# Optimization experiments

Measured on AMD Instinct MI355X. Metric: run time of the kernel, lower is better.

## Reference

```python
import jax, jax.numpy as jnp
import numpy as np
from functools import reduce

N_QUBITS = 6
DIM = 2 ** N_QUBITS  # 64

# PauliZ expectation signs per wire: zsign[j, q] = +1 if bit q of basis state j is 0 else -1
# PennyLane convention: wire 0 is the most-significant bit.
_ZSIGN = jnp.asarray(1.0 - 2.0 * ((np.arange(DIM)[:, None] >> (N_QUBITS - 1 - np.arange(N_QUBITS))[None, :]) & 1), dtype=jnp.float32)  # [64, 6]

def _cnot_perm(c, t):
    # permutation p with new_state[j] = old_state[p[j]] for CNOT(control=c, target=t)
    idx = np.arange(DIM)
    cbit = (idx >> (N_QUBITS - 1 - c)) & 1
    return idx ^ (cbit << (N_QUBITS - 1 - t))

def _ring_perm(r):
    # compose the ring of CNOTs: CNOT(w, (w+r)%n) for w = 0..n-1 applied in order
    total = np.arange(DIM)
    for w in range(N_QUBITS):
        total = total[_cnot_perm(w, (w + r) % N_QUBITS)]
    return total

_RING = {r: jnp.asarray(_ring_perm(r)) for r in (1, 2)}

def _rot(phi, theta, omega):
    # PennyLane Rot(phi, theta, omega) = RZ(omega) @ RY(theta) @ RZ(phi)
    c = jnp.cos(theta / 2.0)
    s = jnp.sin(theta / 2.0)
    em = jnp.exp(-0.5j * (phi + omega))
    ep = jnp.exp(0.5j * (phi - omega))
    return jnp.stack([jnp.stack([em * c, -ep * s]),
                      jnp.stack([jnp.conj(ep) * s, jnp.conj(em) * c])])

def _strongly_entangling(psi, theta):
    # theta: [L, N_QUBITS, 3]; psi: [B, 64] complex
    L = theta.shape[0]
    for l in range(L):
        mats = [_rot(theta[l, w, 0], theta[l, w, 1], theta[l, w, 2]) for w in range(N_QUBITS)]
        U = reduce(jnp.kron, mats)  # [64, 64]; wire 0 = most significant, matches kron order
        psi = psi @ U.T
        r = l % (N_QUBITS - 1) + 1  # PennyLane default ranges
        psi = psi[:, _RING[r]]
    return psi

def setup_inputs() -> dict:
    key = jax.random.key(0)
    ks = jax.random.split(key, 12)
    B, D, H, NW = 131072, 64, 64, 5
    return {
        'x': jax.random.normal(ks[0], (B, D), dtype=jnp.float32),
        'W1': jax.random.normal(ks[1], (H, D), dtype=jnp.float32) * 0.1,
        'b1': jnp.zeros((H,), dtype=jnp.float32),
        'ln_g': jnp.ones((H,), dtype=jnp.float32),
        'ln_b': jnp.zeros((H,), dtype=jnp.float32),
        'W2': jax.random.normal(ks[2], (N_QUBITS, H), dtype=jnp.float32) * 0.1,
        'b2': jnp.zeros((N_QUBITS,), dtype=jnp.float32),
        'theta_shared': jax.random.normal(ks[3], (2, N_QUBITS, 3), dtype=jnp.float32) * 0.1,
        'theta_task': jax.random.normal(ks[4], (1, N_QUBITS, 3), dtype=jnp.float32) * 0.1,
        'Wc': jax.random.normal(ks[5], (NW, N_QUBITS), dtype=jnp.float32) * 0.1,
        'bc': jnp.zeros((NW,), dtype=jnp.float32),
    }

def reference(x, W1, b1, ln_g, ln_b, W2, b2, theta_shared, theta_task, Wc, bc):
    # --- encoder: Linear -> ReLU -> LayerNorm -> Linear -> Tanh ---
    h = jax.nn.relu(x @ W1.T + b1)
    mu = h.mean(-1, keepdims=True)
    var = ((h - mu) ** 2).mean(-1, keepdims=True)
    h = (h - mu) / jnp.sqrt(var + 1e-5) * ln_g + ln_b
    z = jnp.tanh(h @ W2.T + b2)  # [B, 6], in [-1, 1]
    # --- amplitude prep: RY(pi * z_q) on |0> per qubit -> product state ---
    half = (jnp.pi * z) / 2.0
    vec = jnp.stack([jnp.cos(half), jnp.sin(half)], axis=-1)  # [B, 6, 2]
    psi = vec[:, 0]
    for q in range(1, N_QUBITS):
        psi = (psi[:, :, None] * vec[:, q][:, None, :]).reshape(psi.shape[0], -1)
    psi = psi.astype(jnp.complex64)  # [B, 64]
    # --- VQC layers ---
    psi = _strongly_entangling(psi, theta_shared)
    psi = _strongly_entangling(psi, theta_task)
    # --- PauliZ expectation per wire ---
    probs = (psi * jnp.conj(psi)).real  # [B, 64]
    q_out = probs @ _ZSIGN  # [B, 6]
    # --- linear classifier ---
    return q_out @ Wc.T + bc
```

## Files before the change

### kernel.cpp

```cpp
#include <hip/hip_runtime.h>
#include <utility>

#define NQ 6
#define DIM 64

namespace {

constexpr int ring_entry(int r, int i) {
    int idx = i;
    for (int w = NQ - 1; w >= 0; --w) {
        int c = w;
        int t = (w + r) % NQ;
        int cbit = (idx >> (NQ - 1 - c)) & 1;
        idx ^= cbit << (NQ - 1 - t);
    }
    return idx;
}

constexpr int ring_inv(int r, int j) {
    for (int i = 0; i < DIM; ++i) if (ring_entry(r, i) == j) return i;
    return -1;
}

constexpr int insert_zero(int k, int b) {
    return ((k >> b) << (b + 1)) | (k & ((1 << b) - 1));
}

}

template<int W, int... K>
__device__ __forceinline__ void wire_inlane_impl(float* sr, float* si,
        const float* __restrict__ g, std::integer_sequence<int, K...>) {
    const float u00r = g[0], u00i = g[1], u01r = g[2], u01i = g[3];
    const float u10r = g[4], u10i = g[5], u11r = g[6], u11i = g[7];
    constexpr int b = 5 - W;
    (([&] {
        constexpr int l0 = insert_zero(K, b);
        constexpr int l1 = l0 | (1 << b);
        const float ar = sr[l0], ai = si[l0];
        const float br = sr[l1], bi = si[l1];
        sr[l0] = u00r*ar - u00i*ai + u01r*br - u01i*bi;
        si[l0] = u00r*ai + u00i*ar + u01r*bi + u01i*br;
        sr[l1] = u10r*ar - u10i*ai + u11r*br - u11i*bi;
        si[l1] = u10r*ai + u10i*ar + u11r*bi + u11i*br;
    }()), ...);
}

__device__ __forceinline__ void wire0_cross(float* sr, float* si,
        const float* __restrict__ g, bool par) {
    const float cAr = par ? g[6] : g[0];
    const float cAi = par ? g[7] : g[1];
    const float cBr = par ? g[4] : g[2];
    const float cBi = par ? g[5] : g[3];
#pragma unroll
    for (int l = 0; l < 32; ++l) {
        const float mr = sr[l], mi = si[l];
        const float tr = __shfl_xor(mr, 1, 64);
        const float ti = __shfl_xor(mi, 1, 64);
        sr[l] = cAr*mr - cAi*mi + cBr*tr - cBi*ti;
        si[l] = cAr*mi + cAi*mr + cBr*ti + cBi*tr;
    }
}

__device__ __forceinline__ void layer(float* sr, float* si,
        const float* __restrict__ g, bool par) {
    wire0_cross(sr, si, g, par);
    wire_inlane_impl<1>(sr, si, g + 8,  std::make_integer_sequence<int, 16>{});
    wire_inlane_impl<2>(sr, si, g + 16, std::make_integer_sequence<int, 16>{});
    wire_inlane_impl<3>(sr, si, g + 24, std::make_integer_sequence<int, 16>{});
    wire_inlane_impl<4>(sr, si, g + 32, std::make_integer_sequence<int, 16>{});
    wire_inlane_impl<5>(sr, si, g + 40, std::make_integer_sequence<int, 16>{});
}

template<int R, int... L>
__device__ __forceinline__ void ring_impl(float* sr, float* si, bool par,
                                          std::integer_sequence<int, L...>) {
    constexpr int C = ring_entry(R, 32);
    static_assert(((C >> 5) & 1) == 1, "lane-crossing structure assumed");
    constexpr int d = C & 31;
    float nr[32], ni[32];
    (([&] {
        constexpr int ql = ring_entry(R, L);
        constexpr int a  = ql & 31;
        constexpr bool cross = (ql >> 5) & 1;
        if constexpr (cross) {
            const float er = par ? sr[a] : sr[a ^ d];
            const float ei = par ? si[a] : si[a ^ d];
            nr[L] = __shfl_xor(er, 1, 64);
            ni[L] = __shfl_xor(ei, 1, 64);
        } else {
            nr[L] = par ? sr[a ^ d] : sr[a];
            ni[L] = par ? si[a ^ d] : si[a];
        }
    }()), ...);
    (((sr[L] = nr[L]), (si[L] = ni[L])), ...);
}

template<int... L>
__device__ __forceinline__ void readout_impl(const float* sr, const float* si, float* q,
                                             std::integer_sequence<int, L...>) {
    (([&] {
        constexpr int inv = ring_inv(1, L);
        const float pb = sr[L]*sr[L] + si[L]*si[L];
        q[0] += ((inv >> 5) & 1) ? -pb : pb;
        q[1] += ((inv >> 4) & 1) ? -pb : pb;
        q[2] += ((inv >> 3) & 1) ? -pb : pb;
        q[3] += ((inv >> 2) & 1) ? -pb : pb;
        q[4] += ((inv >> 1) & 1) ? -pb : pb;
        q[5] += ( inv       & 1) ? -pb : pb;
    }()), ...);
}

__device__ __forceinline__ void compute_gates6(const float* __restrict__ th, float* g) {
#pragma unroll
    for (int w = 0; w < NQ; ++w) {
        const float phi = th[w*3+0], theta = th[w*3+1], omega = th[w*3+2];
        float s, c, sa, ca, sb, cb;
        __sincosf(0.5f * theta, &s, &c);
        __sincosf(0.5f * (phi + omega), &sa, &ca);
        __sincosf(0.5f * (phi - omega), &sb, &cb);
        g[w*8+0] =  ca * c;  g[w*8+1] = -sa * c;
        g[w*8+2] = -cb * s;  g[w*8+3] = -sb * s;
        g[w*8+4] =  cb * s;  g[w*8+5] = -sb * s;
        g[w*8+6] =  ca * c;  g[w*8+7] =  sa * c;
    }
}

__global__ void setup_kernel(const float* __restrict__ th_s, const float* __restrict__ th_t,
                             const float* __restrict__ ln_g, const float* __restrict__ ln_b,
                             const float* __restrict__ W2, const float* __restrict__ b2,
                             float* __restrict__ ws) {
    const int t = threadIdx.x;
    if (t < 18) {
        const int l = t / 6, w = t % 6;
        const float* th = (l < 2) ? (th_s + (l * 6 + w) * 3) : (th_t + w * 3);
        const float phi = th[0], theta = th[1], omega = th[2];
        float s, c, sa, ca, sb, cb;
        sincosf(0.5f * theta, &s, &c);
        sincosf(0.5f * (phi + omega), &sa, &ca);
        sincosf(0.5f * (phi - omega), &sb, &cb);
        float* g = ws + t * 8;
        g[0] =  ca * c;  g[1] = -sa * c;
        g[2] = -cb * s;  g[3] = -sb * s;
        g[4] =  cb * s;  g[5] = -sb * s;
        g[6] =  ca * c;  g[7] =  sa * c;
    }
    if (t < 384) {
        const int j = t / 6, m = t % 6;
        ws[144 + t] = ln_g[j] * W2[m * 64 + j];
    }
    if (t < 6) {
        float c1 = 0.f, c2 = 0.f;
        for (int j = 0; j < 64; ++j) {
            c1 += ln_g[j] * W2[t * 64 + j];
            c2 += ln_b[j] * W2[t * 64 + j];
        }
        ws[528 + t] = c1;
        ws[534 + t] = c2 + b2[t];
    }
}

template<bool USE_WS>
__global__ __launch_bounds__(256, 4)
void qmaml_kernel(
    const float* __restrict__ x,  const float* __restrict__ W1, const float* __restrict__ b1,
    const float* __restrict__ ln_g, const float* __restrict__ ln_b,
    const float* __restrict__ W2, const float* __restrict__ b2,
    const float* __restrict__ th_s, const float* __restrict__ th_t,
    const float* __restrict__ Wc, const float* __restrict__ bc,
    const float* __restrict__ ws, float* __restrict__ out, int nrows) {

    const int t   = blockIdx.x * 256 + threadIdx.x;
    const int row = t >> 1;
    const bool par = t & 1;
    if (row >= nrows) return;

    float4 xv[16];
    const float4* xp = (const float4*)(x + (long)row * 64);
#pragma unroll
    for (int k = 0; k < 16; ++k) xv[k] = xp[k];

    float A[6]  = {0.f, 0.f, 0.f, 0.f, 0.f, 0.f};
    float C1[6] = {0.f, 0.f, 0.f, 0.f, 0.f, 0.f};
    float C2[6] = {0.f, 0.f, 0.f, 0.f, 0.f, 0.f};
    float s = 0.f, s2 = 0.f;

    for (int j = 0; j < 64; ++j) {
        const float4* wr = (const float4*)(W1 + j * 64);
        float acc = b1[j];
#pragma unroll
        for (int k = 0; k < 16; ++k) {
            const float4 w4 = wr[k];
            acc = fmaf(w4.x, xv[k].x, acc);
            acc = fmaf(w4.y, xv[k].y, acc);
            acc = fmaf(w4.z, xv[k].z, acc);
            acc = fmaf(w4.w, xv[k].w, acc);
        }
        acc = fmaxf(acc, 0.f);
        s += acc; s2 += acc * acc;
        if constexpr (USE_WS) {
            const float* Gt = ws + 144 + j * 6;
#pragma unroll
            for (int m = 0; m < 6; ++m) A[m] = fmaf(acc, Gt[m], A[m]);
        } else {
            const float gj = ln_g[j], bj = ln_b[j];
#pragma unroll
            for (int m = 0; m < 6; ++m) {
                const float w2 = W2[m * 64 + j];
                const float gw = gj * w2;
                A[m]  = fmaf(acc, gw, A[m]);
                C1[m] += gw;
                C2[m] = fmaf(bj, w2, C2[m]);
            }
        }
    }

    const float mu  = s  * (1.f / 64.f);
    const float var = s2 * (1.f / 64.f) - mu * mu;
    const float inv = rsqrtf(var + 1e-5f);

    float vc[6], vsn[6];
#pragma unroll
    for (int m = 0; m < 6; ++m) {
        float c1v, c2v;
        if constexpr (USE_WS) { c1v = ws[528 + m]; c2v = ws[534 + m]; }
        else                  { c1v = C1[m];       c2v = C2[m] + b2[m]; }
        const float zp = inv * (A[m] - mu * c1v) + c2v;
        const float e  = __expf(2.f * zp);
        const float z  = 1.f - 2.f / (e + 1.f);
        const float half = 1.57079632679f * z;
        vsn[m] = __sinf(half);
        vc[m]  = __cosf(half);
    }

    float gf[48];
    const float* g0;
    if constexpr (USE_WS) g0 = ws;
    else { compute_gates6(th_s, gf); g0 = gf; }

    float gar[6], gai[6], gbr[6], gbi[6];
#pragma unroll
    for (int w = 0; w < 6; ++w) {
        const float c = vc[w], sv = vsn[w];
        gar[w] = g0[w*8+0]*c + g0[w*8+2]*sv;
        gai[w] = g0[w*8+1]*c + g0[w*8+3]*sv;
        gbr[w] = g0[w*8+4]*c + g0[w*8+6]*sv;
        gbi[w] = g0[w*8+5]*c + g0[w*8+7]*sv;
    }

    float c1r_[2], c1i_[2];
    {
        const float c0r = par ? gbr[0] : gar[0];
        const float c0i = par ? gbi[0] : gai[0];
#pragma unroll
        for (int k = 0; k < 2; ++k) {
            const float yr = k ? gbr[1] : gar[1], yi = k ? gbi[1] : gai[1];
            c1r_[k] = c0r * yr - c0i * yi;
            c1i_[k] = c0r * yi + c0i * yr;
        }
    }
    float c2r_[4], c2i_[4];
#pragma unroll
    for (int k = 0; k < 4; ++k) {
        const int h = k >> 1, b = k & 1;
        const float yr = b ? gbr[2] : gar[2], yi = b ? gbi[2] : gai[2];
        c2r_[k] = c1r_[h] * yr - c1i_[h] * yi;
        c2i_[k] = c1r_[h] * yi + c1i_[h] * yr;
    }
    float c3r[8], c3i[8];
#pragma unroll
    for (int k = 0; k < 8; ++k) {
        const int h = k >> 1, b = k & 1;
        const float yr = b ? gbr[3] : gar[3], yi = b ? gbi[3] : gai[3];
        c3r[k] = c2r_[h] * yr - c2i_[h] * yi;
        c3i[k] = c2r_[h] * yi + c2i_[h] * yr;
    }
    float c4r[16], c4i[16];
#pragma unroll
    for (int k = 0; k < 16; ++k) {
        const int h = k >> 1, b = k & 1;
        const float yr = b ? gbr[4] : gar[4], yi = b ? gbi[4] : gai[4];
        c4r[k] = c3r[h] * yr - c3i[h] * yi;
        c4i[k] = c3r[h] * yi + c3i[h] * yr;
    }
    float sr[32], si[32];
#pragma unroll
    for (int k = 0; k < 32; ++k) {
        const int h = k >> 1, b = k & 1;
        const float yr = b ? gbr[5] : gar[5], yi = b ? gbi[5] : gai[5];
        sr[k] = c4r[h] * yr - c4i[h] * yi;
        si[k] = c4r[h] * yi + c4i[h] * yr;
    }

    ring_impl<1>(sr, si, par, std::make_integer_sequence<int, 32>{});
    if constexpr (USE_WS) {
        layer(sr, si, ws + 48, par);
        ring_impl<2>(sr, si, par, std::make_integer_sequence<int, 32>{});
        layer(sr, si, ws + 96, par);
    } else {
        compute_gates6(th_s + 18, gf);
        layer(sr, si, gf, par);
        ring_impl<2>(sr, si, par, std::make_integer_sequence<int, 32>{});
        compute_gates6(th_t, gf);
        layer(sr, si, gf, par);
    }

    float q[6] = {0.f, 0.f, 0.f, 0.f, 0.f, 0.f};
    readout_impl(sr, si, q, std::make_integer_sequence<int, 32>{});

    const float pm = par ? -1.f : 1.f;
    constexpr int invC = ring_inv(1, 32);
#pragma unroll
    for (int w = 0; w < 6; ++w) {
        float tq = q[w];
        if ((invC >> (5 - w)) & 1) tq *= pm;
        q[w] = tq + __shfl_xor(tq, 1, 64);
    }

    float o[5];
#pragma unroll
    for (int n = 0; n < 5; ++n) {
        float v = bc[n];
#pragma unroll
        for (int w = 0; w < 6; ++w) v = fmaf(q[w], Wc[n * 6 + w], v);
        o[n] = v;
    }
    float* orow = out + (long)row * 5;
    if (!par) { orow[0] = o[0]; orow[1] = o[1]; orow[2] = o[2]; }
    else      { orow[3] = o[3]; orow[4] = o[4]; }
}

extern "C" void kernel_launch(void* const* d_in, const int* in_sizes, int n_in,
                              void* d_out, int out_size, void* d_ws, size_t ws_size,
                              hipStream_t stream) {
    const float* x   = (const float*)d_in[0];
    const float* W1  = (const float*)d_in[1];
    const float* b1  = (const float*)d_in[2];
    const float* lng = (const float*)d_in[3];
    const float* lnb = (const float*)d_in[4];
    const float* W2  = (const float*)d_in[5];
    const float* b2  = (const float*)d_in[6];
    const float* ths = (const float*)d_in[7];
    const float* tht = (const float*)d_in[8];
    const float* Wc  = (const float*)d_in[9];
    const float* bc  = (const float*)d_in[10];
    float* out = (float*)d_out;
    float* ws  = (float*)d_ws;

    const int nrows = in_sizes[0] / 64;
    const int nthreads = nrows * 2;
    const int grid = (nthreads + 255) / 256;

    if (ws_size >= 540 * sizeof(float)) {
        setup_kernel<<<1, 384, 0, stream>>>(ths, tht, lng, lnb, W2, b2, ws);
        qmaml_kernel<true><<<grid, 256, 0, stream>>>(x, W1, b1, lng, lnb, W2, b2,
                                                     ths, tht, Wc, bc, ws, out, nrows);
    } else {
        qmaml_kernel<false><<<grid, 256, 0, stream>>>(x, W1, b1, lng, lnb, W2, b2,
                                                      ths, tht, Wc, bc, nullptr, out, nrows);
    }
}
```

Baseline: 157.6 us.

## Fold CNOT ring permutations into index maps and use DPP lane swaps

Instead of physically permuting the statevector registers after each CNOT ring, the kernel tracks the accumulated permutation at compile time and applies each single-qubit gate directly through the permuted index mapping, choosing per-pair coefficients by parity. This drops the register shuffles and cross-lane exchanges that the explicit ring permutations needed. Cross-lane exchanges also switch from __shfl_xor to a DPP quad-permute move, which avoids LDS-based shuffles. The price is more complex compile-time index logic and some gates now needing a lane swap where they were purely in-lane before.

```diff
diff --git a/kernel.cpp b/kernel.cpp
--- a/kernel.cpp
+++ b/kernel.cpp
@@ -17,97 +17,144 @@
     return idx;
 }
 
-constexpr int ring_inv(int r, int j) {
-    for (int i = 0; i < DIM; ++i) if (ring_entry(r, i) == j) return i;
+constexpr int Mc(int L, int i) {
+    if (L == 1) return ring_entry(1, i);
+    if (L == 2) return ring_entry(1, ring_entry(2, i));
+    if (L == 3) return ring_entry(1, ring_entry(2, ring_entry(1, i)));
+    return i;
+}
+
+constexpr int Minv(int L, int p) {
+    for (int i = 0; i < DIM; ++i) if (Mc(L, i) == p) return i;
     return -1;
 }
 
-constexpr int insert_zero(int k, int b) {
-    return ((k >> b) << (b + 1)) | (k & ((1 << b) - 1));
-}
-
-}
-
-template<int W, int... K>
-__device__ __forceinline__ void wire_inlane_impl(float* sr, float* si,
-        const float* __restrict__ g, std::integer_sequence<int, K...>) {
-    const float u00r = g[0], u00i = g[1], u01r = g[2], u01i = g[3];
-    const float u10r = g[4], u10i = g[5], u11r = g[6], u11i = g[7];
-    constexpr int b = 5 - W;
+}
+
+__device__ __forceinline__ float swap1(float v) {
+    return __int_as_float(__builtin_amdgcn_mov_dpp(__float_as_int(v), 0xB1, 0xF, 0xF, true));
+}
+
+
+template<int LY, int W, int d, int... Ls>
+__device__ __forceinline__ void wire_inlane(float* sr, float* si,
+        float A0r, float A0i, float B0r, float B0i,
+        float A1r, float A1i, float B1r, float B1i,
+        std::integer_sequence<int, Ls...>) {
     (([&] {
-        constexpr int l0 = insert_zero(K, b);
-        constexpr int l1 = l0 | (1 << b);
-        const float ar = sr[l0], ai = si[l0];
-        const float br = sr[l1], bi = si[l1];
-        sr[l0] = u00r*ar - u00i*ai + u01r*br - u01i*bi;
-        si[l0] = u00r*ai + u00i*ar + u01r*bi + u01i*br;
-        sr[l1] = u10r*ar - u10i*ai + u11r*br - u11i*bi;
-        si[l1] = u10r*ai + u10i*ar + u11r*bi + u11i*br;
+        if constexpr (Ls < (Ls ^ d)) {
+            constexpr int la = Ls, lb = Ls ^ d;
+            constexpr int ra = (Minv(LY, la) >> (5 - W)) & 1;
+            constexpr int rb = (Minv(LY, lb) >> (5 - W)) & 1;
+            const float cAar = ra ? A1r : A0r, cAai = ra ? A1i : A0i;
+            const float cBar = ra ? B1r : B0r, cBai = ra ? B1i : B0i;
+            const float cAbr = rb ? A1r : A0r, cAbi = rb ? A1i : A0i;
+            const float cBbr = rb ? B1r : B0r, cBbi = rb ? B1i : B0i;
+            const float mar = sr[la], mai = si[la];
+            const float mbr = sr[lb], mbi = si[lb];
+            sr[la] = cAar*mar - cAai*mai + cBar*mbr - cBai*mbi;
+            si[la] = cAar*mai + cAai*mar + cBar*mbi + cBai*mbr;
+            sr[lb] = cAbr*mbr - cAbi*mbi + cBbr*mar - cBbi*mai;
+            si[lb] = cAbr*mbi + cAbi*mbr + cBbr*mai + cBbi*mar;
+        }
     }()), ...);
 }
 
-__device__ __forceinline__ void wire0_cross(float* sr, float* si,
+template<int LY, int W, int... Ls>
+__device__ __forceinline__ void wire_cross0(float* sr, float* si,
+        float A0r, float A0i, float B0r, float B0i,
+        float A1r, float A1i, float B1r, float B1i,
+        std::integer_sequence<int, Ls...>) {
+    (([&] {
+        constexpr int r = (Minv(LY, Ls) >> (5 - W)) & 1;
+        const float cAr = r ? A1r : A0r, cAi = r ? A1i : A0i;
+        const float cBr = r ? B1r : B0r, cBi = r ? B1i : B0i;
+        const float mr = sr[Ls], mi = si[Ls];
+        const float tr = swap1(mr), ti = swap1(mi);
+        sr[Ls] = cAr*mr - cAi*mi + cBr*tr - cBi*ti;
+        si[Ls] = cAr*mi + cAi*mr + cBr*ti + cBi*tr;
+    }()), ...);
+}
+
+template<int LY, int W, int d, int... Ls>
+__device__ __forceinline__ void wire_crossd(float* sr, float* si,
+        float A0r, float A0i, float B0r, float B0i,
+        float A1r, float A1i, float B1r, float B1i,
+        std::integer_sequence<int, Ls...>) {
+    (([&] {
+        if constexpr (Ls < (Ls ^ d)) {
+            constexpr int la = Ls, lb = Ls ^ d;
+            constexpr int ra = (Minv(LY, la) >> (5 - W)) & 1;
+            constexpr int rb = (Minv(LY, lb) >> (5 - W)) & 1;
+            const float cAar = ra ? A1r : A0r, cAai = ra ? A1i : A0i;
+            const float cBar = ra ? B1r : B0r, cBai = ra ? B1i : B0i;
+            const float cAbr = rb ? A1r : A0r, cAbi = rb ? A1i : A0i;
+            const float cBbr = rb ? B1r : B0r, cBbi = rb ? B1i : B0i;
+            const float mar = sr[la], mai = si[la];
+            const float mbr = sr[lb], mbi = si[lb];
+            const float tar = swap1(mbr), tai_ = swap1(mbi);
+            const float tbr = swap1(mar), tbi_ = swap1(mai);
+            sr[la] = cAar*mar - cAai*mai + cBar*tar - cBai*tai_;
+            si[la] = cAar*mai + cAai*mar + cBar*tai_ + cBai*tar;
+            sr[lb] = cAbr*mbr - cAbi*mbi + cBbr*tbr - cBbi*tbi_;
+            si[lb] = cAbr*mbi + cAbi*mbr + cBbr*tbi_ + cBbi*tbr;
+        }
+    }()), ...);
+}
+
+template<int LY, int W>
+__device__ __forceinline__ void wire_apply(float* sr, float* si,
         const float* __restrict__ g, bool par) {
-    const float cAr = par ? g[6] : g[0];
-    const float cAi = par ? g[7] : g[1];
-    const float cBr = par ? g[4] : g[2];
-    const float cBi = par ? g[5] : g[3];
-#pragma unroll
-    for (int l = 0; l < 32; ++l) {
-        const float mr = sr[l], mi = si[l];
-        const float tr = __shfl_xor(mr, 1, 64);
-        const float ti = __shfl_xor(mi, 1, 64);
-        sr[l] = cAr*mr - cAi*mi + cBr*tr - cBi*ti;
-        si[l] = cAr*mi + cAi*mr + cBr*ti + cBi*tr;
-    }
-}
-
-__device__ __forceinline__ void layer(float* sr, float* si,
+    constexpr int D = Mc(LY, 1 << (5 - W));
+    constexpr bool cross = (D >> 5) & 1;
+    constexpr int d = D & 31;
+    constexpr bool cpar = (Minv(LY, 32) >> (5 - W)) & 1;
+
+    float A0r, A0i, B0r, B0i, A1r, A1i, B1r, B1i;
+    if constexpr (cpar) {
+        A0r = par ? g[6] : g[0];  A0i = par ? g[7] : g[1];
+        B0r = par ? g[4] : g[2];  B0i = par ? g[5] : g[3];
+        A1r = par ? g[0] : g[6];  A1i = par ? g[1] : g[7];
+        B1r = par ? g[2] : g[4];  B1i = par ? g[3] : g[5];
+    } else {
+        A0r = g[0]; A0i = g[1]; B0r = g[2]; B0i = g[3];
+        A1r = g[6]; A1i = g[7]; B1r = g[4]; B1i = g[5];
+    }
+    if constexpr (!cross) {
+        wire_inlane<LY, W, d>(sr, si, A0r, A0i, B0r, B0i, A1r, A1i, B1r, B1i,
+                              std::make_integer_sequence<int, 32>{});
+    } else if constexpr (d == 0) {
+        wire_cross0<LY, W>(sr, si, A0r, A0i, B0r, B0i, A1r, A1i, B1r, B1i,
+                           std::make_integer_sequence<int, 32>{});
+    } else {
+        wire_crossd<LY, W, d>(sr, si, A0r, A0i, B0r, B0i, A1r, A1i, B1r, B1i,
+                              std::make_integer_sequence<int, 32>{});
+    }
+}
+
+template<int LY>
+__device__ __forceinline__ void layer_apply(float* sr, float* si,
         const float* __restrict__ g, bool par) {
-    wire0_cross(sr, si, g, par);
-    wire_inlane_impl<1>(sr, si, g + 8,  std::make_integer_sequence<int, 16>{});
-    wire_inlane_impl<2>(sr, si, g + 16, std::make_integer_sequence<int, 16>{});
-    wire_inlane_impl<3>(sr, si, g + 24, std::make_integer_sequence<int, 16>{});
-    wire_inlane_impl<4>(sr, si, g + 32, std::make_integer_sequence<int, 16>{});
-    wire_inlane_impl<5>(sr, si, g + 40, std::make_integer_sequence<int, 16>{});
-}
-
-template<int R, int... L>
-__device__ __forceinline__ void ring_impl(float* sr, float* si, bool par,
-                                          std::integer_sequence<int, L...>) {
-    constexpr int C = ring_entry(R, 32);
-    static_assert(((C >> 5) & 1) == 1, "lane-crossing structure assumed");
-    constexpr int d = C & 31;
-    float nr[32], ni[32];
+    wire_apply<LY, 0>(sr, si, g,      par);
+    wire_apply<LY, 1>(sr, si, g + 8,  par);
+    wire_apply<LY, 2>(sr, si, g + 16, par);
+    wire_apply<LY, 3>(sr, si, g + 24, par);
+    wire_apply<LY, 4>(sr, si, g + 32, par);
+    wire_apply<LY, 5>(sr, si, g + 40, par);
+}
+
+template<int... Ls>
+__device__ __forceinline__ void readout_impl(const float* sr, const float* si, float* q,
+                                             std::integer_sequence<int, Ls...>) {
     (([&] {
-        constexpr int ql = ring_entry(R, L);
-        constexpr int a  = ql & 31;
-        constexpr bool cross = (ql >> 5) & 1;
-        if constexpr (cross) {
-            const float er = par ? sr[a] : sr[a ^ d];
-            const float ei = par ? si[a] : si[a ^ d];
-            nr[L] = __shfl_xor(er, 1, 64);
-            ni[L] = __shfl_xor(ei, 1, 64);
-        } else {
-            nr[L] = par ? sr[a ^ d] : sr[a];
-            ni[L] = par ? si[a ^ d] : si[a];
-        }
-    }()), ...);
-    (((sr[L] = nr[L]), (si[L] = ni[L])), ...);
-}
-
-template<int... L>
-__device__ __forceinline__ void readout_impl(const float* sr, const float* si, float* q,
-                                             std::integer_sequence<int, L...>) {
-    (([&] {
-        constexpr int inv = ring_inv(1, L);
-        const float pb = sr[L]*sr[L] + si[L]*si[L];
-        q[0] += ((inv >> 5) & 1) ? -pb : pb;
-        q[1] += ((inv >> 4) & 1) ? -pb : pb;
-        q[2] += ((inv >> 3) & 1) ? -pb : pb;
-        q[3] += ((inv >> 2) & 1) ? -pb : pb;
-        q[4] += ((inv >> 1) & 1) ? -pb : pb;
-        q[5] += ( inv       & 1) ? -pb : pb;
+        constexpr int iv = Minv(3, Ls);
+        const float pb = sr[Ls]*sr[Ls] + si[Ls]*si[Ls];
+        q[0] += ((iv >> 5) & 1) ? -pb : pb;
+        q[1] += ((iv >> 4) & 1) ? -pb : pb;
+        q[2] += ((iv >> 3) & 1) ? -pb : pb;
+        q[3] += ((iv >> 2) & 1) ? -pb : pb;
+        q[4] += ((iv >> 1) & 1) ? -pb : pb;
+        q[5] += ( iv       & 1) ? -pb : pb;
     }()), ...);
 }
 
@@ -292,29 +339,26 @@
         si[k] = c4r[h] * yi + c4i[h] * yr;
     }
 
-    ring_impl<1>(sr, si, par, std::make_integer_sequence<int, 32>{});
     if constexpr (USE_WS) {
-        layer(sr, si, ws + 48, par);
-        ring_impl<2>(sr, si, par, std::make_integer_sequence<int, 32>{});
-        layer(sr, si, ws + 96, par);
+        layer_apply<1>(sr, si, ws + 48, par);
+        layer_apply<2>(sr, si, ws + 96, par);
     } else {
         compute_gates6(th_s + 18, gf);
-        layer(sr, si, gf, par);
-        ring_impl<2>(sr, si, par, std::make_integer_sequence<int, 32>{});
+        layer_apply<1>(sr, si, gf, par);
         compute_gates6(th_t, gf);
-        layer(sr, si, gf, par);
+        layer_apply<2>(sr, si, gf, par);
     }
 
     float q[6] = {0.f, 0.f, 0.f, 0.f, 0.f, 0.f};
     readout_impl(sr, si, q, std::make_integer_sequence<int, 32>{});
 
     const float pm = par ? -1.f : 1.f;
-    constexpr int invC = ring_inv(1, 32);
+    constexpr int invC = Minv(3, 32);
 #pragma unroll
     for (int w = 0; w < 6; ++w) {
         float tq = q[w];
         if ((invC >> (5 - w)) & 1) tq *= pm;
-        q[w] = tq + __shfl_xor(tq, 1, 64);
+        q[w] = tq + swap1(tq);
     }
 
     float o[5];
```

Measured after the change: 155.9 us. Within noise of the previous version (-1.1%).
